# Kernel optimization log

Measured on AMD Instinct MI355X. Metric: run time of the kernel, lower is better.

The kernel has to match this reference:

```python
import jax, jax.numpy as jnp
import numpy as np
from jax import lax
from jax.scipy.linalg import solve_triangular

SR = 16000
FRAME_PERIOD = 80
FFT_LENGTH = 1024
WIN_MS = 30
EPS = 1e-05
DEFAULT_F0 = 150.0
B, T, N = 8, 320000, 4000

N_BAND = int(np.log2(SR / 600))  # 4
CUTOFF = [SR / 2 ** i for i in range(2, N_BAND + 1)]
CUTOFF.append(CUTOFF[-1])  # [4000, 2000, 1000, 1000]
SEG = [int(c * WIN_MS / 500 + 1.5) for c in CUTOFF]  # [241, 121, 61, 61]

_HHP_VALS = [0.00041447996898231424, 0.0007812505141729248, -0.0010917236836275842,
             -0.001986792567596759, 0.0020903896961562292, 0.004094057027284935,
             -0.0034025808529816698, -0.007496154127205602, 0.004972263339933064,
             0.012738791249119802, -0.006696032689574911, -0.020694051570247052,
             0.008432436565041345, 0.03307438375870053, -0.010018936738799522,
             -0.05423136140580825, 0.011293988915051487, 0.10020081367388213,
             -0.012120546202484579, -0.316300210390957, 0.5124068258062764]
_HLP_VALS = [-0.0006548817007748305, 7.561994958159384e-05, 0.0020408456937895227,
             -0.0007468053532203044, -0.004350223568826493, 0.0025966428382642732,
             0.007639602282756696, -0.006490411890149785, -0.011765804538954506,
             0.013649908479276255, 0.01636866479016021, -0.026075976030529347,
             -0.020910294856659444, 0.04826072503231665, 0.02476784661104811,
             -0.09617846758336064, -0.027359756709866623, 0.3148805216163004,
             0.5282734359405503]

def _qmf_high():
    h = np.zeros(41)
    h[:21] = _HHP_VALS
    h[21:] = h[19::-1]
    return h.astype(np.float32)

def _qmf_low():
    h = np.zeros(37)
    h[:19] = _HLP_VALS
    h[19:] = h[17::-1]
    return h.astype(np.float32)

def _make_window():
    w = np.zeros((N_BAND, SEG[0]), np.float32)
    for i, s in enumerate(SEG):
        w[i, :s] = np.hanning(s + 2)[1:-1]
    return w

def _interp_tables():
    coarse = np.concatenate([[0.0], [SR / 2 ** i for i in range(N_BAND, 0, -1)]])
    freq = np.arange(FFT_LENGTH // 2 + 1) * (SR / FFT_LENGTH)
    idx = np.clip(np.searchsorted(coarse, freq) - 1, 0, len(coarse) - 2)
    x0 = coarse[:-1]
    dx = coarse[1:] - x0
    wts = ((freq - x0[idx]) / dx[idx]).astype(np.float32)
    return idx.astype(np.int32), wts

_HHP = _qmf_high()
_HLP = _qmf_low()
_WIN = _make_window()
_IDX, _WTS = _interp_tables()


def _qmf_conv(x, h):
    # x: (B, T), h: (k,). Reflection pad k//2, cross-correlation, stride 2.
    p = h.shape[0] // 2
    xp = jnp.pad(x, ((0, 0), (p, p)), mode='reflect')
    out = lax.conv_general_dilated(xp[:, None, :], h[None, None, :], (2,), 'VALID',
                                   dimension_numbers=('NCH', 'OIH', 'NCH'))
    return out[:, 0, :]


def setup_inputs() -> dict:
    key = jax.random.key(0)
    k1, k2 = jax.random.split(key)
    x = jax.random.normal(k1, (B, T), jnp.float32)
    f0 = 100.0 + 200.0 * jax.random.uniform(k2, (B, N), jnp.float32)  # 100-300 Hz
    return {"x": x, "f0": f0}


def reference(x, f0):
    hHP = jnp.asarray(_HHP)
    hLP = jnp.asarray(_HLP)
    f0 = lax.stop_gradient(jnp.where(f0 <= 32, DEFAULT_F0, f0))
    Bn, Nf = f0.shape
    time_axis = jnp.arange(Nf, dtype=f0.dtype) * (FRAME_PERIOD / SR)
    bidx = jnp.arange(Bn)[:, None, None]
    eye6 = EPS * jnp.eye(6, dtype=x.dtype)
    lx = x
    bap = []
    for i in range(N_BAND):
        if i < N_BAND - 1:
            hx = _qmf_conv(lx, hHP)
            lx = _qmf_conv(lx, hLP)
            xb = hx
        else:
            xb = lx
        seg = SEG[i]
        tmp_fs = 2.0 * CUTOFF[i]
        pitch = tmp_fs / f0
        t0 = (pitch + 0.5).astype(jnp.int32)
        index_bias = (pitch * 0.5 + 0.5).astype(jnp.int32)
        curr_pos = (time_axis * tmp_fs + 1.5).astype(jnp.int32)[None, :]
        origin = curr_pos - index_bias  # (B, N)
        j = jnp.arange(-1, seg + 1)  # (seg+2,)
        T1 = xb.shape[-1] - 1
        ia = jnp.clip((origin - t0)[..., None] + j, 0, T1)
        ib = jnp.clip((origin + t0)[..., None] + j, 0, T1)
        Ha = xb[bidx, ia]  # (B, N, seg+2)
        Hb = xb[bidx, ib]

        def unfold3(a):  # size-3 sliding windows -> (B, N, seg, 3)
            return jnp.stack([a[..., 0:seg], a[..., 1:seg + 1], a[..., 2:seg + 2]], axis=-1)

        H = jnp.concatenate([unfold3(Ha), unfold3(Hb)], axis=-1)  # (B, N, seg, 6)
        w = jnp.asarray(_WIN[i, :seg])
        Hw = jnp.swapaxes(H, -2, -1) * w  # (B, N, 6, seg)
        R = Hw @ H  # (B, N, 6, 6)
        ig = jnp.clip(origin[..., None] + j[1:-1], 0, T1)
        X = xb[bidx, ig][..., None]  # (B, N, seg, 1)
        L = jnp.linalg.cholesky(R + eye6)
        b = Hw @ X  # (B, N, 6, 1)
        y1 = solve_triangular(L, b, lower=True)
        a = solve_triangular(jnp.swapaxes(L, -2, -1), y1, lower=False)
        HaX = H @ a  # (B, N, seg, 1)
        wsqrt = jnp.sqrt(w)
        wx = wsqrt * X[..., 0]
        wxHa = wsqrt * (X - HaX)[..., 0]
        A = jnp.std(wxHa, axis=-1, ddof=1) / (jnp.std(wx, axis=-1, ddof=1) + 1e-16)
        bap.append(A)
    bap.append(bap[-1])
    ap = jnp.stack(bap[::-1], axis=-1)  # (B, N, n_band+1), low->high freq
    # piecewise-linear interpolation in log domain onto fft bins
    y = jnp.log(ap)
    y0 = y[..., :-1]
    dy = y[..., 1:] - y0
    yi = jnp.take(dy, jnp.asarray(_IDX), axis=-1) * jnp.asarray(_WTS) \
         + jnp.take(y0, jnp.asarray(_IDX), axis=-1)
    return jnp.exp(yi)  # (B, N, fft//2+1)
```

## Files before the change

kernel.cpp:

```cpp
#include <hip/hip_runtime.h>
#include <math.h>

#define NB 8
#define NF 4000
#define NFRAMES (NB * NF)
#define TOTF (4 * NFRAMES)

__constant__ float c_hhp[21] = {
    0.00041447996898231424, 0.0007812505141729248, -0.0010917236836275842,
    -0.001986792567596759,  0.0020903896961562292, 0.004094057027284935,
    -0.0034025808529816698, -0.007496154127205602, 0.004972263339933064,
    0.012738791249119802,   -0.006696032689574911, -0.020694051570247052,
    0.008432436565041345,   0.03307438375870053,   -0.010018936738799522,
    -0.05423136140580825,   0.011293988915051487,  0.10020081367388213,
    -0.012120546202484579,  -0.316300210390957,    0.5124068258062764};
__constant__ float c_hlp[19] = {
    -0.0006548817007748305, 7.561994958159384e-05, 0.0020408456937895227,
    -0.0007468053532203044, -0.004350223568826493, 0.0025966428382642732,
    0.007639602282756696,   -0.006490411890149785, -0.011765804538954506,
    0.013649908479276255,   0.01636866479016021,   -0.026075976030529347,
    -0.020910294856659444,  0.04826072503231665,   0.02476784661104811,
    -0.09617846758336064,   -0.027359756709866623, 0.3148805216163004,
    0.5282734359405503};

__device__ __forceinline__ int reflidx(int i, int len) {
  if (i < 0) i = -i;
  if (i >= len) i = 2 * len - 2 - i;
  return i;
}
__device__ __forceinline__ int clampi(int i, int hi) {
  return min(max(i, 0), hi);
}
__device__ __forceinline__ float4 ld4(const float* p) {
  return *reinterpret_cast<const float4*>(p);
}

__global__ __launch_bounds__(256) void qmf_kernel(
    const float* __restrict__ in, int len, float* __restrict__ outH,
    float* __restrict__ outL, float2* __restrict__ wtab) {
  int half = len >> 1;
  int gid = blockIdx.x * 256 + threadIdx.x;
  if (gid >= NB * half) {
    if (wtab) {
      const int segs[4] = {241, 121, 61, 61};
      int k = threadIdx.x;
      for (int i = 0; i < 4; ++i) {
        float v = 0.f;
        if (k < segs[i]) {
          double ang = 2.0 * 3.14159265358979323846 * (double)(k + 1) /
                       (double)(segs[i] + 1);
          v = (float)(0.5 - 0.5 * cos(ang));
        }
        wtab[i * 256 + k] = make_float2(v, sqrtf(v));
      }
    }
    return;
  }
  int b = gid / half;
  int nn = gid - b * half;
  const float* row = in + (size_t)b * len;
  int c = 2 * nn;
  float sh = 0.f, sl = 0.f;
  if (c >= 20 && c <= len - 22) {
    const float2* p2 = reinterpret_cast<const float2*>(row + (c - 20));
    float v[42];
#pragma unroll
    for (int j = 0; j < 21; ++j) {
      float2 t = p2[j];
      v[2 * j] = t.x;
      v[2 * j + 1] = t.y;
    }
#pragma unroll
    for (int t = 0; t < 41; ++t) sh += v[t] * c_hhp[t <= 20 ? t : 40 - t];
#pragma unroll
    for (int t = 0; t < 37; ++t) sl += v[t + 2] * c_hlp[t <= 18 ? t : 36 - t];
  } else {
#pragma unroll
    for (int t = 0; t < 41; ++t)
      sh += row[reflidx(c + t - 20, len)] * c_hhp[t <= 20 ? t : 40 - t];
#pragma unroll
    for (int t = 0; t < 37; ++t)
      sl += row[reflidx(c + t - 18, len)] * c_hlp[t <= 18 ? t : 36 - t];
  }
  outH[(size_t)b * half + nn] = sh;
  outL[(size_t)b * half + nn] = sl;
}

__device__ __forceinline__ void accum1(float wk, float wsk, float h0, float h1,
                                       float h2, float h3, float h4, float h5,
                                       float x, float* __restrict__ rr,
                                       float* __restrict__ bv,
                                       float* __restrict__ gv, float& sxx,
                                       float& s1x) {
  sxx += wk * x * x;
  s1x += wsk * x;
  float wh0 = wk * h0, wh1 = wk * h1, wh2 = wk * h2, wh3 = wk * h3,
        wh4 = wk * h4, wh5 = wk * h5;
  gv[0] += wsk * h0; gv[1] += wsk * h1; gv[2] += wsk * h2;
  gv[3] += wsk * h3; gv[4] += wsk * h4; gv[5] += wsk * h5;
  bv[0] += wh0 * x;  bv[1] += wh1 * x;  bv[2] += wh2 * x;
  bv[3] += wh3 * x;  bv[4] += wh4 * x;  bv[5] += wh5 * x;
  rr[0] += wh0 * h0;  rr[1] += wh0 * h1;  rr[2] += wh0 * h2;
  rr[3] += wh0 * h3;  rr[4] += wh0 * h4;  rr[5] += wh0 * h5;
  rr[6] += wh1 * h1;  rr[7] += wh1 * h2;  rr[8] += wh1 * h3;
  rr[9] += wh1 * h4;  rr[10] += wh1 * h5; rr[11] += wh2 * h2;
  rr[12] += wh2 * h3; rr[13] += wh2 * h4; rr[14] += wh2 * h5;
  rr[15] += wh3 * h3; rr[16] += wh3 * h4; rr[17] += wh3 * h5;
  rr[18] += wh4 * h4; rr[19] += wh4 * h5; rr[20] += wh5 * h5;
}

template <int GS, int NITER, bool CLAMP>
__device__ __forceinline__ void acc_loop(
    const float* __restrict__ row, int T1, int base_a, int base_b, int origin,
    int sub, const float2* __restrict__ wtab, float rr[21], float bv[6],
    float gv[6], float& sxx, float& s1x) {
  if (!CLAMP) {
    const float* pa = row + base_a + 4 * sub;
    const float* pb = row + base_b + 4 * sub;
    const float* pg = row + origin + 4 * sub;
    const float* pw = reinterpret_cast<const float*>(wtab + 4 * sub);
#pragma unroll 2
    for (int j = 0; j < NITER; ++j) {
      const int off = j * 4 * GS;
      float4 a0 = ld4(pa + off);
      float4 a1 = ld4(pa + off + 4);
      float4 b0 = ld4(pb + off);
      float4 b1 = ld4(pb + off + 4);
      float4 xx = ld4(pg + off);
      float4 w01 = ld4(pw + 2 * off);
      float4 w23 = ld4(pw + 2 * off + 4);
      accum1(w01.x, w01.y, a0.x, a0.y, a0.z, b0.x, b0.y, b0.z, xx.x, rr, bv,
             gv, sxx, s1x);
      accum1(w01.z, w01.w, a0.y, a0.z, a0.w, b0.y, b0.z, b0.w, xx.y, rr, bv,
             gv, sxx, s1x);
      accum1(w23.x, w23.y, a0.z, a0.w, a1.x, b0.z, b0.w, b1.x, xx.z, rr, bv,
             gv, sxx, s1x);
      accum1(w23.z, w23.w, a0.w, a1.x, a1.y, b0.w, b1.x, b1.y, xx.w, rr, bv,
             gv, sxx, s1x);
    }
  } else {
#pragma unroll 2
    for (int j = 0; j < NITER; ++j) {
#pragma unroll
      for (int m = 0; m < 4; ++m) {
        int k = 4 * (sub + j * GS) + m;
        float2 wp = wtab[k];
        int ia = base_a + k, ib = base_b + k;
        float h0 = row[clampi(ia, T1)];
        float h1 = row[clampi(ia + 1, T1)];
        float h2 = row[clampi(ia + 2, T1)];
        float h3 = row[clampi(ib, T1)];
        float h4 = row[clampi(ib + 1, T1)];
        float h5 = row[clampi(ib + 2, T1)];
        float x = row[clampi(origin + k, T1)];
        accum1(wp.x, wp.y, h0, h1, h2, h3, h4, h5, x, rr, bv, gv, sxx, s1x);
      }
    }
  }
}

template <int SEG, int LGS, int NITER>
__device__ __forceinline__ void band_body(
    const float* __restrict__ xb, int bandLen, const float* __restrict__ f0,
    float tmp_fs, const float2* __restrict__ wtab, float* __restrict__ sums_col,
    int blk) {
  constexpr int GS = 1 << LGS;
  constexpr int FPB = 256 / GS;
  constexpr int KMAX = 4 * GS * NITER;
  const int tid = threadIdx.x;
  const int sub = tid & (GS - 1);
  const int frame = blk * FPB + (tid >> LGS);
  const int b = frame / NF;
  const int n = frame - b * NF;

  float f0v = f0[frame];
  if (f0v <= 32.0f) f0v = 150.0f;
  float pitch = tmp_fs / f0v;
  int t0 = (int)(__fadd_rn(pitch, 0.5f));
  int ibias = (int)(__fadd_rn(__fmul_rn(pitch, 0.5f), 0.5f));
  float tt = __fmul_rn((float)n, 0.005f);
  int curr = (int)(__fadd_rn(__fmul_rn(tt, tmp_fs), 1.5f));
  int origin = curr - ibias;
  const int T1 = bandLen - 1;
  const float* row = xb + (size_t)b * bandLen;
  const int base_a = origin - t0 - 1;
  const int base_b = origin + t0 - 1;

  float rr[21], bv[6], gv[6], sxx = 0.f, s1x = 0.f;
#pragma unroll
  for (int i = 0; i < 21; ++i) rr[i] = 0.f;
#pragma unroll
  for (int i = 0; i < 6; ++i) bv[i] = 0.f;
#pragma unroll
  for (int i = 0; i < 6; ++i) gv[i] = 0.f;

  const bool fast = (base_a >= 0) && (base_b + KMAX + 3 <= T1);
  if (fast)
    acc_loop<GS, NITER, false>(row, T1, base_a, base_b, origin, sub, wtab, rr,
                               bv, gv, sxx, s1x);
  else
    acc_loop<GS, NITER, true>(row, T1, base_a, base_b, origin, sub, wtab, rr,
                              bv, gv, sxx, s1x);

#pragma unroll
  for (int off = GS / 2; off >= 1; off >>= 1) {
#pragma unroll
    for (int i = 0; i < 21; ++i) rr[i] += __shfl_xor(rr[i], off, 64);
#pragma unroll
    for (int i = 0; i < 6; ++i) bv[i] += __shfl_xor(bv[i], off, 64);
#pragma unroll
    for (int i = 0; i < 6; ++i) gv[i] += __shfl_xor(gv[i], off, 64);
    sxx += __shfl_xor(sxx, off, 64);
    s1x += __shfl_xor(s1x, off, 64);
  }

  if (sub == 0) {
    float* sp = sums_col + frame;
#pragma unroll
    for (int i = 0; i < 21; ++i) sp[(size_t)i * TOTF] = rr[i];
#pragma unroll
    for (int i = 0; i < 6; ++i) sp[(size_t)(21 + i) * TOTF] = bv[i];
#pragma unroll
    for (int i = 0; i < 6; ++i) sp[(size_t)(27 + i) * TOTF] = gv[i];
    sp[(size_t)33 * TOTF] = sxx;
    sp[(size_t)34 * TOTF] = s1x;
  }
}

__global__ __launch_bounds__(256) void bands_kernel(
    const float* __restrict__ hx0, const float* __restrict__ hx1,
    const float* __restrict__ hx2, const float* __restrict__ lx2,
    const float* __restrict__ f0, const float2* __restrict__ wtab,
    float* __restrict__ sums) {
  int blk = blockIdx.x;
  if (blk < 1000) {
    band_body<241, 3, 8>(hx0, 160000, f0, 8000.0f, wtab + 0 * 256,
                         sums + 0 * NFRAMES, blk);
  } else if (blk < 2000) {
    band_body<121, 3, 4>(hx1, 80000, f0, 4000.0f, wtab + 1 * 256,
                         sums + 1 * NFRAMES, blk - 1000);
  } else if (blk < 2500) {
    band_body<61, 2, 4>(hx2, 40000, f0, 2000.0f, wtab + 2 * 256,
                        sums + 2 * NFRAMES, blk - 2000);
  } else {
    band_body<61, 2, 4>(lx2, 40000, f0, 2000.0f, wtab + 3 * 256,
                        sums + 3 * NFRAMES, blk - 2500);
  }
}

__global__ __launch_bounds__(256) void solve_kernel(
    const float* __restrict__ sums, float* __restrict__ Aarr) {
  const int t = blockIdx.x * 256 + threadIdx.x;
  float v[35];
#pragma unroll
  for (int i = 0; i < 35; ++i) v[i] = sums[(size_t)i * TOTF + t];
  const float nf = (t >= 2 * NFRAMES) ? 61.0f
                   : (t >= NFRAMES)   ? 121.0f
                                      : 241.0f;
  float sxx = v[33], s1x = v[34];

  float M[6][6], invd[6];
  {
    int c = 0;
#pragma unroll
    for (int p = 0; p < 6; ++p)
#pragma unroll
      for (int q = p; q < 6; ++q) {
        M[p][q] = v[c];
        M[q][p] = v[c];
        ++c;
      }
#pragma unroll
    for (int p = 0; p < 6; ++p) M[p][p] += 1e-5f;
  }
#pragma unroll
  for (int p = 0; p < 6; ++p) {
    float d = M[p][p];
#pragma unroll
    for (int j = 0; j < 6; ++j)
      if (j < p) d -= M[p][j] * M[p][j];
    d = sqrtf(d);
    M[p][p] = d;
    float inv = 1.0f / d;
    invd[p] = inv;
#pragma unroll
    for (int q = 0; q < 6; ++q)
      if (q > p) {
        float s = M[q][p];
#pragma unroll
        for (int j = 0; j < 6; ++j)
          if (j < p) s -= M[q][j] * M[p][j];
        M[q][p] = s * inv;
      }
  }
  float yv[6], av[6];
#pragma unroll
  for (int p = 0; p < 6; ++p) {
    float s = v[21 + p];
#pragma unroll
    for (int j = 0; j < 6; ++j)
      if (j < p) s -= M[p][j] * yv[j];
    yv[p] = s * invd[p];
  }
#pragma unroll
  for (int p = 5; p >= 0; --p) {
    float s = yv[p];
#pragma unroll
    for (int j = 0; j < 6; ++j)
      if (j > p) s -= M[j][p] * av[j];
    av[p] = s * invd[p];
  }

  float adotb = 0.f, adotg = 0.f, quad = 0.f;
  {
    int c = 0;
#pragma unroll
    for (int p = 0; p < 6; ++p) {
      adotb += av[p] * v[21 + p];
      adotg += av[p] * v[27 + p];
#pragma unroll
      for (int q = p; q < 6; ++q) {
        float tt = av[p] * av[q] * v[c++];
        quad += (q == p) ? tt : 2.f * tt;
      }
    }
  }
  float s2r = sxx - 2.f * adotb + quad;
  float s1r = s1x - adotg;
  float vx = (sxx - s1x * s1x / nf) / (nf - 1.0f);
  float vr = (s2r - s1r * s1r / nf) / (nf - 1.0f);
  float sx = sqrtf(fmaxf(vx, 0.f));
  float sr = sqrtf(fmaxf(vr, 0.f));
  Aarr[t] = sr / (sx + 1e-16f);
}

__global__ __launch_bounds__(256) void interp_kernel(
    const float* __restrict__ A, float* __restrict__ out) {
  const int wave = threadIdx.x >> 6;
  const int lane = threadIdx.x & 63;
  const int f = blockIdx.x * 4 + wave;
  float l0 = __logf(A[0 * NFRAMES + f]);
  float l1 = __logf(A[1 * NFRAMES + f]);
  float l2 = __logf(A[2 * NFRAMES + f]);
  float l3 = __logf(A[3 * NFRAMES + f]);
  float d1 = l2 - l3, d2 = l1 - l2, d3 = l0 - l1;
  float* orow = out + (size_t)f * 513;
  for (int k = lane; k < 513; k += 64) {
    float y0, dy, c;
    int k0;
    if (k <= 64) {
      y0 = l3; dy = 0.f; k0 = 0; c = 0.015625f;
    } else if (k <= 128) {
      y0 = l3; dy = d1; k0 = 64; c = 0.015625f;
    } else if (k <= 256) {
      y0 = l2; dy = d2; k0 = 128; c = 0.0078125f;
    } else {
      y0 = l1; dy = d3; k0 = 256; c = 0.00390625f;
    }
    float w = (float)(k - k0) * c;
    orow[k] = __expf(y0 + w * dy);
  }
}

extern "C" void kernel_launch(void* const* d_in, const int* in_sizes, int n_in,
                              void* d_out, int out_size, void* d_ws,
                              size_t ws_size, hipStream_t stream) {
  const float* x = (const float*)d_in[0];
  const float* f0 = (const float*)d_in[1];
  float* out = (float*)d_out;
  float* ws = (float*)d_ws;

  float* hx0 = ws + 0;
  float* lx0 = hx0 + 1280000;
  float* hx1 = lx0 + 1280000;
  float* lx1 = hx1 + 640000;
  float* hx2 = lx1 + 640000;
  float* lx2 = hx2 + 320000;
  float* Aarr = lx2 + 320000;
  float2* wtab = (float2*)(Aarr + 4 * NFRAMES);
  float* sums = (float*)(wtab + 4 * 256);
  (void)ws_size;

  hipLaunchKernelGGL(qmf_kernel, dim3(5000), dim3(256), 0, stream, x, 320000,
                     hx0, lx0, (float2*)nullptr);
  hipLaunchKernelGGL(qmf_kernel, dim3(2500), dim3(256), 0, stream, lx0,
                     160000, hx1, lx1, (float2*)nullptr);
  hipLaunchKernelGGL(qmf_kernel, dim3(1251), dim3(256), 0, stream, lx1, 80000,
                     hx2, lx2, wtab);

  hipLaunchKernelGGL(bands_kernel, dim3(3000), dim3(256), 0, stream, hx0, hx1,
                     hx2, lx2, f0, wtab, sums);

  hipLaunchKernelGGL(solve_kernel, dim3(TOTF / 256), dim3(256), 0, stream,
                     sums, Aarr);

  hipLaunchKernelGGL(interp_kernel, dim3(NFRAMES / 4), dim3(256), 0, stream,
                     Aarr, out);
}
```

Baseline: 80.75 us.

## Fuse Cholesky solve into band accumulation kernel and vectorize interp stores

The per-frame 6x6 Cholesky solve and the variance ratio move into the band kernel, so the 35-column sums buffer is never written to or read back from global memory and one launch goes away. The gv reduction is replaced by reducing only the dot product a·g across the subgroup, and every lane in the group redoes the small solve. The interp kernel now has each lane write 8 contiguous bins with two float4 stores and handles bin 512 separately. The cost is redundant solve arithmetic in all GS lanes and higher register pressure in the band kernel.

```diff
diff --git a/kernel.cpp b/kernel.cpp
--- a/kernel.cpp
+++ b/kernel.cpp
@@ -4,7 +4,6 @@
 #define NB 8
 #define NF 4000
 #define NFRAMES (NB * NF)
-#define TOTF (4 * NFRAMES)
 
 __constant__ float c_hhp[21] = {
     0.00041447996898231424, 0.0007812505141729248, -0.0010917236836275842,
@@ -33,6 +32,9 @@
 }
 __device__ __forceinline__ float4 ld4(const float* p) {
   return *reinterpret_cast<const float4*>(p);
+}
+__device__ __forceinline__ void st4(float* p, float4 v) {
+  *reinterpret_cast<float4*>(p) = v;
 }
 
 __global__ __launch_bounds__(256) void qmf_kernel(
@@ -162,7 +164,7 @@
 template <int SEG, int LGS, int NITER>
 __device__ __forceinline__ void band_body(
     const float* __restrict__ xb, int bandLen, const float* __restrict__ f0,
-    float tmp_fs, const float2* __restrict__ wtab, float* __restrict__ sums_col,
+    float tmp_fs, const float2* __restrict__ wtab, float* __restrict__ Aout,
     int blk) {
   constexpr int GS = 1 << LGS;
   constexpr int FPB = 256 / GS;
@@ -208,56 +210,9 @@
     for (int i = 0; i < 21; ++i) rr[i] += __shfl_xor(rr[i], off, 64);
 #pragma unroll
     for (int i = 0; i < 6; ++i) bv[i] += __shfl_xor(bv[i], off, 64);
-#pragma unroll
-    for (int i = 0; i < 6; ++i) gv[i] += __shfl_xor(gv[i], off, 64);
     sxx += __shfl_xor(sxx, off, 64);
     s1x += __shfl_xor(s1x, off, 64);
   }
-
-  if (sub == 0) {
-    float* sp = sums_col + frame;
-#pragma unroll
-    for (int i = 0; i < 21; ++i) sp[(size_t)i * TOTF] = rr[i];
-#pragma unroll
-    for (int i = 0; i < 6; ++i) sp[(size_t)(21 + i) * TOTF] = bv[i];
-#pragma unroll
-    for (int i = 0; i < 6; ++i) sp[(size_t)(27 + i) * TOTF] = gv[i];
-    sp[(size_t)33 * TOTF] = sxx;
-    sp[(size_t)34 * TOTF] = s1x;
-  }
-}
-
-__global__ __launch_bounds__(256) void bands_kernel(
-    const float* __restrict__ hx0, const float* __restrict__ hx1,
-    const float* __restrict__ hx2, const float* __restrict__ lx2,
-    const float* __restrict__ f0, const float2* __restrict__ wtab,
-    float* __restrict__ sums) {
-  int blk = blockIdx.x;
-  if (blk < 1000) {
-    band_body<241, 3, 8>(hx0, 160000, f0, 8000.0f, wtab + 0 * 256,
-                         sums + 0 * NFRAMES, blk);
-  } else if (blk < 2000) {
-    band_body<121, 3, 4>(hx1, 80000, f0, 4000.0f, wtab + 1 * 256,
-                         sums + 1 * NFRAMES, blk - 1000);
-  } else if (blk < 2500) {
-    band_body<61, 2, 4>(hx2, 40000, f0, 2000.0f, wtab + 2 * 256,
-                        sums + 2 * NFRAMES, blk - 2000);
-  } else {
-    band_body<61, 2, 4>(lx2, 40000, f0, 2000.0f, wtab + 3 * 256,
-                        sums + 3 * NFRAMES, blk - 2500);
-  }
-}
-
-__global__ __launch_bounds__(256) void solve_kernel(
-    const float* __restrict__ sums, float* __restrict__ Aarr) {
-  const int t = blockIdx.x * 256 + threadIdx.x;
-  float v[35];
-#pragma unroll
-  for (int i = 0; i < 35; ++i) v[i] = sums[(size_t)i * TOTF + t];
-  const float nf = (t >= 2 * NFRAMES) ? 61.0f
-                   : (t >= NFRAMES)   ? 121.0f
-                                      : 241.0f;
-  float sxx = v[33], s1x = v[34];
 
   float M[6][6], invd[6];
   {
@@ -266,8 +221,8 @@
     for (int p = 0; p < 6; ++p)
 #pragma unroll
       for (int q = p; q < 6; ++q) {
-        M[p][q] = v[c];
-        M[q][p] = v[c];
+        M[p][q] = rr[c];
+        M[q][p] = rr[c];
         ++c;
       }
 #pragma unroll
@@ -296,7 +251,7 @@
   float yv[6], av[6];
 #pragma unroll
   for (int p = 0; p < 6; ++p) {
-    float s = v[21 + p];
+    float s = bv[p];
 #pragma unroll
     for (int j = 0; j < 6; ++j)
       if (j < p) s -= M[p][j] * yv[j];
@@ -311,27 +266,56 @@
     av[p] = s * invd[p];
   }
 
-  float adotb = 0.f, adotg = 0.f, quad = 0.f;
+  float adotg = av[0] * gv[0] + av[1] * gv[1] + av[2] * gv[2] +
+                av[3] * gv[3] + av[4] * gv[4] + av[5] * gv[5];
+#pragma unroll
+  for (int off = GS / 2; off >= 1; off >>= 1)
+    adotg += __shfl_xor(adotg, off, 64);
+
+  float adotb = 0.f, quad = 0.f;
   {
     int c = 0;
 #pragma unroll
     for (int p = 0; p < 6; ++p) {
-      adotb += av[p] * v[21 + p];
-      adotg += av[p] * v[27 + p];
+      adotb += av[p] * bv[p];
 #pragma unroll
       for (int q = p; q < 6; ++q) {
-        float tt = av[p] * av[q] * v[c++];
-        quad += (q == p) ? tt : 2.f * tt;
-      }
-    }
-  }
-  float s2r = sxx - 2.f * adotb + quad;
-  float s1r = s1x - adotg;
-  float vx = (sxx - s1x * s1x / nf) / (nf - 1.0f);
-  float vr = (s2r - s1r * s1r / nf) / (nf - 1.0f);
-  float sx = sqrtf(fmaxf(vx, 0.f));
-  float sr = sqrtf(fmaxf(vr, 0.f));
-  Aarr[t] = sr / (sx + 1e-16f);
+        float t = av[p] * av[q] * rr[c++];
+        quad += (q == p) ? t : 2.f * t;
+      }
+    }
+  }
+  if (sub == 0) {
+    float s2r = sxx - 2.f * adotb + quad;
+    float s1r = s1x - adotg;
+    const float nf = (float)SEG;
+    float vx = (sxx - s1x * s1x / nf) / (nf - 1.0f);
+    float vr = (s2r - s1r * s1r / nf) / (nf - 1.0f);
+    float sx = sqrtf(fmaxf(vx, 0.f));
+    float sr = sqrtf(fmaxf(vr, 0.f));
+    Aout[frame] = sr / (sx + 1e-16f);
+  }
+}
+
+__global__ __launch_bounds__(256) void bands_kernel(
+    const float* __restrict__ hx0, const float* __restrict__ hx1,
+    const float* __restrict__ hx2, const float* __restrict__ lx2,
+    const float* __restrict__ f0, const float2* __restrict__ wtab,
+    float* __restrict__ Aarr) {
+  int blk = blockIdx.x;
+  if (blk < 1000) {
+    band_body<241, 3, 8>(hx0, 160000, f0, 8000.0f, wtab + 0 * 256,
+                         Aarr + 0 * NFRAMES, blk);
+  } else if (blk < 2000) {
+    band_body<121, 3, 4>(hx1, 80000, f0, 4000.0f, wtab + 1 * 256,
+                         Aarr + 1 * NFRAMES, blk - 1000);
+  } else if (blk < 2500) {
+    band_body<61, 2, 4>(hx2, 40000, f0, 2000.0f, wtab + 2 * 256,
+                        Aarr + 2 * NFRAMES, blk - 2000);
+  } else {
+    band_body<61, 2, 4>(lx2, 40000, f0, 2000.0f, wtab + 3 * 256,
+                        Aarr + 3 * NFRAMES, blk - 2500);
+  }
 }
 
 __global__ __launch_bounds__(256) void interp_kernel(
@@ -345,7 +329,10 @@
   float l3 = __logf(A[3 * NFRAMES + f]);
   float d1 = l2 - l3, d2 = l1 - l2, d3 = l0 - l1;
   float* orow = out + (size_t)f * 513;
-  for (int k = lane; k < 513; k += 64) {
+  float vals[8];
+#pragma unroll
+  for (int m = 0; m < 8; ++m) {
+    int k = 8 * lane + m;
     float y0, dy, c;
     int k0;
     if (k <= 64) {
@@ -358,8 +345,11 @@
       y0 = l1; dy = d3; k0 = 256; c = 0.00390625f;
     }
     float w = (float)(k - k0) * c;
-    orow[k] = __expf(y0 + w * dy);
-  }
+    vals[m] = __expf(y0 + w * dy);
+  }
+  st4(orow + 8 * lane, make_float4(vals[0], vals[1], vals[2], vals[3]));
+  st4(orow + 8 * lane + 4, make_float4(vals[4], vals[5], vals[6], vals[7]));
+  if (lane == 0) orow[512] = __expf(l1 + d3);
 }
 
 extern "C" void kernel_launch(void* const* d_in, const int* in_sizes, int n_in,
@@ -378,7 +368,6 @@
   float* lx2 = hx2 + 320000;
   float* Aarr = lx2 + 320000;
   float2* wtab = (float2*)(Aarr + 4 * NFRAMES);
-  float* sums = (float*)(wtab + 4 * 256);
   (void)ws_size;
 
   hipLaunchKernelGGL(qmf_kernel, dim3(5000), dim3(256), 0, stream, x, 320000,
@@ -389,10 +378,7 @@
                      hx2, lx2, wtab);
 
   hipLaunchKernelGGL(bands_kernel, dim3(3000), dim3(256), 0, stream, hx0, hx1,
-                     hx2, lx2, f0, wtab, sums);
-
-  hipLaunchKernelGGL(solve_kernel, dim3(TOTF / 256), dim3(256), 0, stream,
-                     sums, Aarr);
+                     hx2, lx2, f0, wtab, Aarr);
 
   hipLaunchKernelGGL(interp_kernel, dim3(NFRAMES / 4), dim3(256), 0, stream,
                      Aarr, out);
```

New measurement: 80.17 us. About the same (-0.7%).
